# Optimization experiments

Hardware: AMD Instinct MI355X
Metric: run time of the kernel (lower is better)

The kernel has to match this reference:

```python
import jax, jax.numpy as jnp
import numpy as np

B, N, K = 16, 2048, 20


def setup_inputs() -> dict:
    key = jax.random.key(0)
    k1, k2 = jax.random.split(key)
    A = jax.random.normal(k1, (B, N, N), dtype=jnp.float32)
    dope = jax.random.uniform(k2, (B, N, N), dtype=jnp.float32)
    return {"A": A, "dope": dope}


def reference(A, dope):
    # act='relu'
    A = jax.nn.relu(A)
    # k-NN sparsification: topk along last dim of randomly doped A
    _, topk_idx = jax.lax.top_k(A + dope * 1e-4, K)  # (B, N, K)
    b_idx = jnp.arange(B)[:, None, None]
    n_idx = jnp.arange(N)[None, :, None]
    mask = jnp.zeros_like(A).at[b_idx, n_idx, topk_idx].set(1.0)
    A = A * mask
    # norm='sym': A <- D^{-1/2} (A + I) D^{-1/2}; diag matmul == broadcast scale
    A = A + jnp.eye(N, dtype=A.dtype)
    d_inv = jnp.sum(A, axis=2) ** -0.5  # (B, N)
    d_inv = jnp.where(jnp.isinf(d_inv), 0.0, d_inv)
    return d_inv[:, :, None] * A * d_inv[:, None, :]
```

## Files before the change

kernel.cpp:

```cpp
#include <hip/hip_runtime.h>


static constexpr int N    = 2048;
static constexpr int KSEL = 20;
static constexpr int NR   = 16 * 2048;

typedef unsigned int uint2v __attribute__((ext_vector_type(2)));
typedef float f32x4 __attribute__((ext_vector_type(4)));

#if __has_builtin(__builtin_nontemporal_load)
#define NT_LOAD(p) __builtin_nontemporal_load(p)
#else
#define NT_LOAD(p) (*(p))
#endif
#if __has_builtin(__builtin_nontemporal_store)
#define NT_STORE(v, p) __builtin_nontemporal_store((v), (p))
#else
#define NT_STORE(v, p) (*(p) = (v))
#endif

#if __has_builtin(__builtin_amdgcn_mov_dpp)
#define XD(v, ctrl) ((unsigned)__builtin_amdgcn_mov_dpp((int)(v), (ctrl), 0xF, 0xF, false))
#else
#define XD(v, ctrl) ((unsigned)__shfl_xor((int)(v), ((ctrl) == 0xB1 ? 1 : 2)))
#endif
#if __has_builtin(__builtin_amdgcn_ds_swizzle)
#define XS(v, imm) ((unsigned)__builtin_amdgcn_ds_swizzle((int)(v), (imm)))
#else
#define XS(v, imm) ((unsigned)__shfl_xor((int)(v), (((imm) >> 10) & 0x1F)))
#endif

__device__ __forceinline__ unsigned read_lane_u32(unsigned v, int srclane) {
#if __has_builtin(__builtin_amdgcn_readlane)
  return (unsigned)__builtin_amdgcn_readlane((int)v, srclane);
#else
  return (unsigned)__shfl((int)v, srclane, 64);
#endif
}

__device__ __forceinline__ void cex(unsigned& hi, unsigned& lo,
                                    unsigned Ahi, unsigned Alo,
                                    unsigned Bhi, unsigned Blo, bool km) {
  unsigned long long Av = ((unsigned long long)Ahi << 32) | Alo;
  unsigned long long Bv = ((unsigned long long)Bhi << 32) | Blo;
  bool sel = (km == (Av > Bv));
  hi = sel ? Ahi : Bhi;
  lo = sel ? Alo : Blo;
}

#define KM(K2, J) ((((lane & (J)) == 0)) != (((lane & (K2)) != 0)))
#define EX1(K2)  cex(hi, lo, hi, lo, XD(hi, 0xB1), XD(lo, 0xB1), KM(K2, 1))
#define EX2(K2)  cex(hi, lo, hi, lo, XD(hi, 0x4E), XD(lo, 0x4E), KM(K2, 2))
#define EX4(K2)  cex(hi, lo, hi, lo, XS(hi, 0x101F), XS(lo, 0x101F), KM(K2, 4))
#define EX8(K2)  cex(hi, lo, hi, lo, XS(hi, 0x201F), XS(lo, 0x201F), KM(K2, 8))
#if __has_builtin(__builtin_amdgcn_permlane16_swap)
#define EX16(K2) { uint2v r_ = __builtin_amdgcn_permlane16_swap(hi, hi, false, false); \
                   uint2v s_ = __builtin_amdgcn_permlane16_swap(lo, lo, false, false); \
                   cex(hi, lo, (unsigned)r_[0], (unsigned)s_[0], (unsigned)r_[1], (unsigned)s_[1], KM(K2, 16)); }
#else
#define EX16(K2) cex(hi, lo, hi, lo, (unsigned)__shfl_xor((int)hi, 16), (unsigned)__shfl_xor((int)lo, 16), KM(K2, 16))
#endif
#if __has_builtin(__builtin_amdgcn_permlane32_swap)
#define EX32(K2) { uint2v r_ = __builtin_amdgcn_permlane32_swap(hi, hi, false, false); \
                   uint2v s_ = __builtin_amdgcn_permlane32_swap(lo, lo, false, false); \
                   cex(hi, lo, (unsigned)r_[0], (unsigned)s_[0], (unsigned)r_[1], (unsigned)s_[1], KM(K2, 32)); }
#else
#define EX32(K2) cex(hi, lo, hi, lo, (unsigned)__shfl_xor((int)hi, 32), (unsigned)__shfl_xor((int)lo, 32), KM(K2, 32))
#endif

__device__ __forceinline__ void ins4(float vc, int jc,
                                     float& t0, float& t1, float& t2, float& t3,
                                     int& j0, int& j1, int& j2, int& j3) {
  bool b0 = vc > t0;
  float d0 = b0 ? t0 : vc; int e0 = b0 ? j0 : jc;
  t0 = b0 ? vc : t0;       j0 = b0 ? jc : j0;
  bool b1 = d0 > t1;
  float d1 = b1 ? t1 : d0; int e1 = b1 ? j1 : e0;
  t1 = b1 ? d0 : t1;       j1 = b1 ? e0 : j1;
  bool b2 = d1 > t2;
  float d2 = b2 ? t2 : d1; int e2 = b2 ? j2 : e1;
  t2 = b2 ? d1 : t2;       j2 = b2 ? e1 : j2;
  bool b3 = d2 > t3;
  t3 = b3 ? d2 : t3;       j3 = b3 ? e2 : j3;
}

__device__ __forceinline__ int wave_topk_exact(const float* __restrict__ Arow,
                                               const float* __restrict__ Drow,
                                               int lane) {
  float v[32];
  const float4* A4 = reinterpret_cast<const float4*>(Arow);
  const float4* D4 = reinterpret_cast<const float4*>(Drow);
#pragma unroll
  for (int c4 = 0; c4 < 8; ++c4) {
    float4 a = A4[c4 * 64 + lane];
    float4 d = D4[c4 * 64 + lane];
    v[c4 * 4 + 0] = __fadd_rn(fmaxf(a.x, 0.0f), __fmul_rn(d.x, 1e-4f));
    v[c4 * 4 + 1] = __fadd_rn(fmaxf(a.y, 0.0f), __fmul_rn(d.y, 1e-4f));
    v[c4 * 4 + 2] = __fadd_rn(fmaxf(a.z, 0.0f), __fmul_rn(d.z, 1e-4f));
    v[c4 * 4 + 3] = __fadd_rn(fmaxf(a.w, 0.0f), __fmul_rn(d.w, 1e-4f));
  }
  float t0 = -1.f, t1 = -1.f, t2 = -1.f, t3 = -1.f;
  int   j0 = 0,    j1 = 0,    j2 = 0,    j3 = 0;
#pragma unroll
  for (int c = 0; c < 32; ++c) {
    int jc = ((c >> 2) << 8) | (lane << 2) | (c & 3);
    ins4(v[c], jc, t0, t1, t2, t3, j0, j1, j2, j3);
  }
  unsigned consumed = 0;
  int jmine = 0;
#pragma unroll 1
  for (int it = 0; it < KSEL; ++it) {
    if (__any(t0 < 0.0f)) {
      if (t0 < 0.0f) {
        t0 = t1 = t2 = t3 = -1.f; j0 = j1 = j2 = j3 = 0;
#pragma unroll
        for (int c = 0; c < 32; ++c) {
          float vc = ((consumed >> c) & 1u) ? -1.0f : v[c];
          int jc = ((c >> 2) << 8) | (lane << 2) | (c & 3);
          ins4(vc, jc, t0, t1, t2, t3, j0, j1, j2, j3);
        }
      }
    }
    float m = t0;
#pragma unroll
    for (int off = 32; off; off >>= 1) m = fmaxf(m, __shfl_xor(m, off));
    int cj = (t0 == m) ? j0 : 0x7fffffff;
#pragma unroll
    for (int off = 32; off; off >>= 1) cj = min(cj, __shfl_xor(cj, off));
    if (lane == it) jmine = cj;
    if (((cj >> 2) & 63) == lane) {
      int c = ((cj >> 8) << 2) | (cj & 3);
      consumed |= (1u << c);
      t0 = t1; j0 = j1; t1 = t2; j1 = j2; t2 = t3; j2 = j3; t3 = -1.f; j3 = 0;
    }
  }
  return jmine;
}

__global__ void __launch_bounds__(256)
topk_fast(const float* __restrict__ A, const float* __restrict__ D,
          float* __restrict__ wval, int* __restrict__ widx,
          float* __restrict__ wdinv) {
  __shared__ unsigned long long cand[4][64];
  __shared__ unsigned scnt[4];
  const float T = 2.05f;
  int lane = threadIdx.x & 63;
  int w = threadIdx.x >> 6;
  int r = blockIdx.x * 4 + w;
  size_t base = (size_t)r * N;
  const f32x4* A4 = reinterpret_cast<const f32x4*>(A + base);

  f32x4 a0 = NT_LOAD(A4 + lane);       f32x4 a1 = NT_LOAD(A4 + 64 + lane);
  f32x4 a2 = NT_LOAD(A4 + 128 + lane); f32x4 a3 = NT_LOAD(A4 + 192 + lane);
  f32x4 a4 = NT_LOAD(A4 + 256 + lane); f32x4 a5 = NT_LOAD(A4 + 320 + lane);
  f32x4 a6 = NT_LOAD(A4 + 384 + lane); f32x4 a7 = NT_LOAD(A4 + 448 + lane);

  cand[w][lane] = 0ull;
  if (lane == 0) scnt[w] = 0u;

#define PUSH1(AV, J) do {                                                      \
    float k_ = fmaxf((AV), 0.0f);                                              \
    if (k_ > T) {                                                              \
      unsigned p_ = atomicAdd(&scnt[w], 1u);                                   \
      if (p_ < 64u)                                                            \
        cand[w][p_] = ((unsigned long long)__float_as_uint(k_) << 32) |        \
                      (unsigned)(2047 - (J));                                  \
    }                                                                          \
  } while (0)
#define PUSH4(AA, C4) do {                                                     \
    int jb_ = ((C4) << 8) | (lane << 2);                                       \
    PUSH1(AA.x, jb_ + 0);                                                      \
    PUSH1(AA.y, jb_ + 1);                                                      \
    PUSH1(AA.z, jb_ + 2);                                                      \
    PUSH1(AA.w, jb_ + 3);                                                      \
  } while (0)

  PUSH4(a0, 0); PUSH4(a1, 1); PUSH4(a2, 2); PUSH4(a3, 3);
  PUSH4(a4, 4); PUSH4(a5, 5); PUSH4(a6, 6); PUSH4(a7, 7);
#undef PUSH4
#undef PUSH1

  __asm__ __volatile__("s_waitcnt lgkmcnt(0)" ::: "memory");
  unsigned cnt = scnt[w];
  unsigned long long kv = cand[w][lane];
  unsigned hi = (unsigned)(kv >> 32), lo = (unsigned)kv;

  EX1(2);
  EX2(4);  EX1(4);
  EX4(8);  EX2(8);  EX1(8);
  EX8(16); EX4(16); EX2(16); EX1(16);
  EX16(32); EX8(32); EX4(32); EX2(32); EX1(32);
  EX32(64); EX16(64); EX8(64); EX4(64); EX2(64); EX1(64);

  float a19 = __uint_as_float(read_lane_u32(hi, 19));
  float a20 = __uint_as_float(read_lane_u32(hi, 20));
  bool decided = (a19 > __fadd_rn(a20, 1e-4f)) && (a19 > __fadd_rn(T, 1e-4f));
  bool bad = (cnt < (unsigned)KSEL) || (cnt > 64u) || !decided;

  int jsel = 2047 - (int)lo;
  float val = (lane < KSEL) ? __uint_as_float(hi) : 0.0f;

  if (bad) {
    int jm = wave_topk_exact(A + base, D + base, lane);
    jsel = jm;
    val = (lane < KSEL) ? fmaxf(A[base + jm], 0.0f) : 0.0f;
  }

  float s = val;
#pragma unroll
  for (int off = 32; off; off >>= 1) s += __shfl_xor(s, off);
  float dinv = (float)(1.0 / sqrt(1.0 + (double)s));

  if (lane < KSEL) {
    wval[r * KSEL + lane] = val;
    widx[r * KSEL + lane] = jsel;
  }
  if (lane == 0) wdinv[r] = dinv;
}

__global__ void __launch_bounds__(256)
scatter_reg(const float* __restrict__ wval, const int* __restrict__ widx,
            const float* __restrict__ wdinv, float* __restrict__ out) {
  int r = blockIdx.x;
  int tid = threadIdx.x;
  int i = r & (N - 1);
  int bb = r & ~(N - 1);
  float di = wdinv[r];

  float v0 = 0.f, v1 = 0.f, v2 = 0.f, v3 = 0.f,
        v4 = 0.f, v5 = 0.f, v6 = 0.f, v7 = 0.f;
  if ((i & 255) == tid) {
    float dd = di * di;
    switch (i >> 8) {
      case 0: v0 = dd; break; case 1: v1 = dd; break;
      case 2: v2 = dd; break; case 3: v3 = dd; break;
      case 4: v4 = dd; break; case 5: v5 = dd; break;
      case 6: v6 = dd; break; case 7: v7 = dd; break;
    }
  }
#pragma unroll
  for (int t = 0; t < KSEL; ++t) {
    int j = widx[r * KSEL + t];
    if ((j & 255) == tid) {
      float c = di * wval[r * KSEL + t] * wdinv[bb + j];
      switch (j >> 8) {
        case 0: v0 += c; break; case 1: v1 += c; break;
        case 2: v2 += c; break; case 3: v3 += c; break;
        case 4: v4 += c; break; case 5: v5 += c; break;
        case 6: v6 += c; break; case 7: v7 += c; break;
      }
    }
  }
  float* o = out + (size_t)r * N;
  NT_STORE(v0, o + tid);         NT_STORE(v1, o + 256 + tid);
  NT_STORE(v2, o + 512 + tid);   NT_STORE(v3, o + 768 + tid);
  NT_STORE(v4, o + 1024 + tid);  NT_STORE(v5, o + 1280 + tid);
  NT_STORE(v6, o + 1536 + tid);  NT_STORE(v7, o + 1792 + tid);
}

__global__ void __launch_bounds__(256)
topk_exact_pass1(const float* __restrict__ A, const float* __restrict__ D,
                 float* __restrict__ wdinv) {
  int lane = threadIdx.x & 63;
  int r = blockIdx.x * 4 + (threadIdx.x >> 6);
  size_t base = (size_t)r * N;
  int jm = wave_topk_exact(A + base, D + base, lane);
  float val = 0.0f;
  if (lane < KSEL) val = fmaxf(A[base + jm], 0.0f);
  float s = (lane < KSEL) ? val : 0.0f;
#pragma unroll
  for (int off = 32; off; off >>= 1) s += __shfl_xor(s, off);
  float dinv = (float)(1.0 / sqrt(1.0 + (double)s));
  if (lane == 0) wdinv[r] = dinv;
}

__global__ void __launch_bounds__(256)
fallback_pass2(const float* __restrict__ A, const float* __restrict__ D,
               const float* __restrict__ wdinv, float* __restrict__ out) {
  __shared__ float rows[4][N];
  int lane = threadIdx.x & 63;
  int w = threadIdx.x >> 6;
  int r = blockIdx.x * 4 + w;
  size_t base = (size_t)r * N;
  int i = r & (N - 1);
  int jm = wave_topk_exact(A + base, D + base, lane);
  float val = 0.0f;
  if (lane < KSEL) val = fmaxf(A[base + jm], 0.0f);
  float s = (lane < KSEL) ? val : 0.0f;
#pragma unroll
  for (int off = 32; off; off >>= 1) s += __shfl_xor(s, off);
  float di = (float)(1.0 / sqrt(1.0 + (double)s));
  float4* rv = reinterpret_cast<float4*>(rows[w]);
  float4 z = make_float4(0.f, 0.f, 0.f, 0.f);
#pragma unroll
  for (int q = 0; q < 8; ++q) rv[q * 64 + lane] = z;
  __syncthreads();
  if (lane < KSEL) {
    float dj = wdinv[(r & ~(N - 1)) + jm];
    atomicAdd(&rows[w][jm], di * val * dj);
  } else if (lane == KSEL) {
    atomicAdd(&rows[w][i], di * di);
  }
  __syncthreads();
  float4* o4 = reinterpret_cast<float4*>(out + base);
#pragma unroll
  for (int q = 0; q < 8; ++q) o4[q * 64 + lane] = rv[q * 64 + lane];
}

extern "C" void kernel_launch(void* const* d_in, const int* in_sizes, int n_in,
                              void* d_out, int out_size, void* d_ws, size_t ws_size,
                              hipStream_t stream) {
  const float* A = (const float*)d_in[0];
  const float* D = (const float*)d_in[1];
  float* out = (float*)d_out;
  char* ws = (char*)d_ws;
  size_t off_val  = 0;
  size_t off_idx  = off_val + (size_t)NR * KSEL * sizeof(float);
  size_t off_dinv = off_idx + (size_t)NR * KSEL * sizeof(int);
  size_t total    = off_dinv + (size_t)NR * sizeof(float);
  if (ws_size >= total) {
    float* wval  = (float*)(ws + off_val);
    int*   widx  = (int*)(ws + off_idx);
    float* wdinv = (float*)(ws + off_dinv);
    topk_fast<<<NR / 4, 256, 0, stream>>>(A, D, wval, widx, wdinv);
    scatter_reg<<<NR, 256, 0, stream>>>(wval, widx, wdinv, out);
  } else {
    float* wdinv = (float*)ws;
    topk_exact_pass1<<<NR / 4, 256, 0, stream>>>(A, D, wdinv);
    fallback_pass2<<<NR / 4, 256, 0, stream>>>(A, D, wdinv, out);
  }
}
```

Baseline: 126.8 us.

## Interleave top-k production and scatter across software-pipelined batch chunks

Merges the top-k and scatter kernels into one mixed kernel and splits the rows into four chunks of whole batches. Each launch computes top-k for chunk k while scattering chunk k-1, interleaving producer and consumer blocks in a 2:1 pattern. The aim is to overlap the read-heavy selection pass with the write-heavy output pass and avoid a full-grid serialization point. It costs extra launches and more complex block scheduling, and scatter blocks now loop over 8 rows each.

```diff
diff --git a/kernel.cpp b/kernel.cpp
--- a/kernel.cpp
+++ b/kernel.cpp
@@ -1,9 +1,10 @@
 #include <hip/hip_runtime.h>
 
 
-static constexpr int N    = 2048;
-static constexpr int KSEL = 20;
-static constexpr int NR   = 16 * 2048;
+static constexpr int N      = 2048;
+static constexpr int KSEL   = 20;
+static constexpr int NR     = 16 * 2048;
+static constexpr int SBROWS = 8192;
 
 typedef unsigned int uint2v __attribute__((ext_vector_type(2)));
 typedef float f32x4 __attribute__((ext_vector_type(4)));
@@ -67,6 +68,15 @@
 #else
 #define EX32(K2) cex(hi, lo, hi, lo, (unsigned)__shfl_xor((int)hi, 32), (unsigned)__shfl_xor((int)lo, 32), KM(K2, 32))
 #endif
+
+#define SORT64() do {                                     \
+    EX1(2);                                               \
+    EX2(4);  EX1(4);                                      \
+    EX4(8);  EX2(8);  EX1(8);                             \
+    EX8(16); EX4(16); EX2(16); EX1(16);                   \
+    EX16(32); EX8(32); EX4(32); EX2(32); EX1(32);         \
+    EX32(64); EX16(64); EX8(64); EX4(64); EX2(64); EX1(64); \
+  } while (0)
 
 __device__ __forceinline__ void ins4(float vc, int jc,
                                      float& t0, float& t1, float& t2, float& t3,
@@ -137,16 +147,15 @@
   return jmine;
 }
 
-__global__ void __launch_bounds__(256)
-topk_fast(const float* __restrict__ A, const float* __restrict__ D,
-          float* __restrict__ wval, int* __restrict__ widx,
-          float* __restrict__ wdinv) {
-  __shared__ unsigned long long cand[4][64];
-  __shared__ unsigned scnt[4];
+__device__ __forceinline__ void produce_row(const float* __restrict__ A,
+                                            const float* __restrict__ D,
+                                            float* __restrict__ wval,
+                                            int* __restrict__ widx,
+                                            float* __restrict__ wdinv,
+                                            int r, int lane, int w,
+                                            unsigned long long (*cand)[64],
+                                            unsigned* scnt) {
   const float T = 2.05f;
-  int lane = threadIdx.x & 63;
-  int w = threadIdx.x >> 6;
-  int r = blockIdx.x * 4 + w;
   size_t base = (size_t)r * N;
   const f32x4* A4 = reinterpret_cast<const f32x4*>(A + base);
 
@@ -184,13 +193,7 @@
   unsigned cnt = scnt[w];
   unsigned long long kv = cand[w][lane];
   unsigned hi = (unsigned)(kv >> 32), lo = (unsigned)kv;
-
-  EX1(2);
-  EX2(4);  EX1(4);
-  EX4(8);  EX2(8);  EX1(8);
-  EX8(16); EX4(16); EX2(16); EX1(16);
-  EX16(32); EX8(32); EX4(32); EX2(32); EX1(32);
-  EX32(64); EX16(64); EX8(64); EX4(64); EX2(64); EX1(64);
+  SORT64();
 
   float a19 = __uint_as_float(read_lane_u32(hi, 19));
   float a20 = __uint_as_float(read_lane_u32(hi, 20));
@@ -218,11 +221,11 @@
   if (lane == 0) wdinv[r] = dinv;
 }
 
-__global__ void __launch_bounds__(256)
-scatter_reg(const float* __restrict__ wval, const int* __restrict__ widx,
-            const float* __restrict__ wdinv, float* __restrict__ out) {
-  int r = blockIdx.x;
-  int tid = threadIdx.x;
+__device__ __forceinline__ void scatter_row(const float* __restrict__ wval,
+                                            const int* __restrict__ widx,
+                                            const float* __restrict__ wdinv,
+                                            float* __restrict__ out,
+                                            int r, int tid) {
   int i = r & (N - 1);
   int bb = r & ~(N - 1);
   float di = wdinv[r];
@@ -256,6 +259,33 @@
   NT_STORE(v2, o + 512 + tid);   NT_STORE(v3, o + 768 + tid);
   NT_STORE(v4, o + 1024 + tid);  NT_STORE(v5, o + 1280 + tid);
   NT_STORE(v6, o + 1536 + tid);  NT_STORE(v7, o + 1792 + tid);
+}
+
+__global__ void __launch_bounds__(256)
+mixed(const float* __restrict__ A, const float* __restrict__ D,
+      float* __restrict__ wval, int* __restrict__ widx,
+      float* __restrict__ wdinv, float* __restrict__ out,
+      int prow0, int np4, int srow0, int ns8) {
+  __shared__ unsigned long long cand[4][64];
+  __shared__ unsigned scnt[4];
+  const int tid = threadIdx.x, lane = tid & 63, w = tid >> 6;
+  int g = blockIdx.x;
+  bool prod;
+  int ri;
+  if (ns8 == 0)       { prod = true;  ri = g; }
+  else if (np4 == 0)  { prod = false; ri = g; }
+  else {
+    if ((g % 3) == 2) { prod = false; ri = g / 3; }
+    else              { prod = true;  ri = (g / 3) * 2 + (g % 3); }
+  }
+  if (prod) {
+    int r = prow0 + ri * 4 + w;
+    produce_row(A, D, wval, widx, wdinv, r, lane, w, cand, scnt);
+  } else {
+#pragma unroll 1
+    for (int k = 0; k < 8; ++k)
+      scatter_row(wval, widx, wdinv, out, srow0 + ri * 8 + k, tid);
+  }
 }
 
 __global__ void __launch_bounds__(256)
@@ -322,8 +352,13 @@
     float* wval  = (float*)(ws + off_val);
     int*   widx  = (int*)(ws + off_idx);
     float* wdinv = (float*)(ws + off_dinv);
-    topk_fast<<<NR / 4, 256, 0, stream>>>(A, D, wval, widx, wdinv);
-    scatter_reg<<<NR, 256, 0, stream>>>(wval, widx, wdinv, out);
+    const int NP = SBROWS / 4;
+    const int NS = SBROWS / 8;
+    mixed<<<NP, 256, 0, stream>>>(A, D, wval, widx, wdinv, out, 0, NP, 0, 0);
+    for (int k = 1; k < 4; ++k)
+      mixed<<<NP + NS, 256, 0, stream>>>(A, D, wval, widx, wdinv, out,
+                                         k * SBROWS, NP, (k - 1) * SBROWS, NS);
+    mixed<<<NS, 256, 0, stream>>>(A, D, wval, widx, wdinv, out, 0, 0, 3 * SBROWS, NS);
   } else {
     float* wdinv = (float*)ws;
     topk_exact_pass1<<<NR / 4, 256, 0, stream>>>(A, D, wdinv);
```

Result: slower. 178.3 us (+40.6%).
